# Performance work log

Measured on AMD Instinct MI355X. Metric: run time of the kernel, lower is better.

Reference implementation:

```python
import jax, jax.numpy as jnp
import numpy as np

DK = 8.0          # sqrt(in_dim) with in_dim = 64
BN_SCALE = 1.0 / np.float32(np.sqrt(1.0 + 1e-5))  # eval-mode BatchNorm3d at init (mean=0, var=1, gamma=1, beta=0)


def conv3d(x, w, b):
    # x: [B,Cin,D1,D2,D3], w: [Cout,Cin,3,3,3], stride 1, padding 1 == SAME
    y = jax.lax.conv_general_dilated(
        x, w, window_strides=(1, 1, 1), padding='SAME',
        dimension_numbers=('NCDHW', 'OIDHW', 'NCDHW'))
    return y + b[None, :, None, None, None]


def axial(qm, km, vm):
    # qm/km/vm: [B,C,S,L,M]; attention over L with keys along M-contraction.
    # scores[b,c,s,i,j] = sum_m (q/dk)[...,i,m] * k[...,j,m]  -> [B,C,S,L,L]
    s = jnp.einsum('bcsim,bcsjm->bcsij', qm / DK, km)
    # torch nn.Softmax(dim=1) applied to [N,L,L] normalizes over the FIRST L axis (i)
    a = jax.nn.softmax(s, axis=-2)
    return jnp.einsum('bcsij,bcsjm->bcsim', a, vm)


def setup_inputs() -> dict:
    key = jax.random.key(0)
    ks = jax.random.split(key, 5)
    B, C, H, W, D = 2, 64, 64, 64, 64
    x = jax.random.normal(ks[0], (B, C, H, W, D), jnp.float32)
    Wq = jax.random.normal(ks[1], (C, C, 3, 3, 3), jnp.float32) * 0.02
    Wk = jax.random.normal(ks[2], (C, C, 3, 3, 3), jnp.float32) * 0.02
    Wv = jax.random.normal(ks[3], (C, C, 3, 3, 3), jnp.float32) * 0.02
    Wc = jax.random.normal(ks[4], (C, 3 * C, 3, 3, 3), jnp.float32) * 0.02
    z = jnp.zeros((C,), jnp.float32)
    return {"x": x, "Wq": Wq, "bq": z, "Wk": Wk, "bk": z,
            "Wv": Wv, "bv": z, "Wc": Wc, "bc": z}


def reference(x, Wq, bq, Wk, bk, Wv, bv, Wc, bc):
    # projections (dropout is inactive at inference)
    q = conv3d(x, Wq, bq)
    k = conv3d(x, Wk, bk)
    v = conv3d(x, Wv, bv)
    P = jnp.transpose

    # ---- loop over D slices: attend over H (and over W in the transposed pass) ----
    pa = (0, 1, 4, 2, 3)        # [B,C,D,H,W]
    ava = axial(P(q, pa), P(k, pa), P(v, pa))          # [B,C,D,H,W]
    ava = P(ava, (0, 1, 3, 4, 2))                       # -> [B,C,H,W,D]
    pb = (0, 1, 4, 3, 2)        # [B,C,D,W,H]
    ava1 = axial(P(q, pb), P(k, pb), P(v, pb))          # [B,C,D,W,H]
    ava1 = P(ava1, (0, 1, 4, 3, 2))                     # -> [B,C,H,W,D]
    AVa = (ava + ava1) * 0.5

    # ---- loop over W slices: attend over H (and over D) ----
    pc = (0, 1, 3, 2, 4)        # [B,C,W,H,D]
    avb = axial(P(q, pc), P(k, pc), P(v, pc))           # [B,C,W,H,D]
    avb = P(avb, (0, 1, 3, 2, 4))                       # -> [B,C,H,W,D]
    pd = (0, 1, 3, 4, 2)        # [B,C,W,D,H]
    avb1 = axial(P(q, pd), P(k, pd), P(v, pd))          # [B,C,W,D,H]
    avb1 = P(avb1, (0, 1, 4, 2, 3))                     # -> [B,C,H,W,D]
    AVb = (avb + avb1) * 0.5

    # ---- loop over H slices: attend over W (and over D) ----
    avc = axial(q, k, v)                                 # [B,C,H,W,D]
    pe = (0, 1, 2, 4, 3)        # [B,C,H,D,W]
    avc1 = axial(P(q, pe), P(k, pe), P(v, pe))          # [B,C,H,D,W]
    avc1 = P(avc1, (0, 1, 2, 4, 3))                     # -> [B,C,H,W,D]
    AVc = (avc + avc1) * 0.5

    cat = jnp.concatenate([AVa, AVb, AVc], axis=1)      # [B,3C,H,W,D]
    y = jax.nn.relu(conv3d(cat, Wc, bc) * BN_SCALE)     # Conv_3x3x3: conv + BN(eval) + ReLU
    y = y * BN_SCALE                                    # outer BatchNorm3d (eval)
    return y + q
```

## Files before the change

kernel.cpp:

```cpp
#include <hip/hip_runtime.h>

typedef unsigned short u16;
typedef unsigned int u32;
typedef __attribute__((ext_vector_type(8))) __bf16 bf16x8;
typedef __attribute__((ext_vector_type(4))) float f32x4;
typedef __attribute__((ext_vector_type(4))) u16 u16x4;

#define VOL 262144

__device__ __forceinline__ u16 f2bf(float f) {
  u32 u = __builtin_bit_cast(u32, f);
  u32 r = u + 0x7FFFu + ((u >> 16) & 1u);
  return (u16)(r >> 16);
}
__device__ __forceinline__ float bf2f(u16 h) {
  return __builtin_bit_cast(float, ((u32)h) << 16);
}
__device__ __forceinline__ bf16x8 ldsfrag(const u16* p) { return *(const bf16x8*)p; }

__global__ __launch_bounds__(256) void swz_qkv(const float* __restrict__ Wq,
    const float* __restrict__ Wk, const float* __restrict__ Wv, u16* __restrict__ out) {
  int idx = blockIdx.x * 256 + threadIdx.x;
  if (idx >= 54 * 12 * 64 * 8) return;
  int jj = idx & 7;
  int lane = (idx >> 3) & 63;
  int t = idx >> 9;
  int nf = t % 12, s = t / 12;
  int dh = s / 18, sub = s % 18;
  int dw = sub / 6, dd = (sub >> 1) % 3, c32 = sub & 1;
  int coutg = nf * 16 + (lane & 15);
  int cin = c32 * 32 + (lane >> 4) * 8 + jj;
  const float* W = (coutg < 64) ? Wq : ((coutg < 128) ? Wk : Wv);
  int c = coutg & 63;
  out[idx] = f2bf(W[(c * 64 + cin) * 27 + dh * 9 + dw * 3 + dd]);
}

__global__ __launch_bounds__(256) void swz_c(const float* __restrict__ Wc, u16* __restrict__ out) {
  int idx = blockIdx.x * 256 + threadIdx.x;
  if (idx >= 162 * 4 * 64 * 8) return;
  int jj = idx & 7;
  int lane = (idx >> 3) & 63;
  int nf = (idx >> 9) & 3;
  int s = idx >> 11;
  int dh = s / 54, rem = s % 54;
  int hf = rem / 27, sub = rem % 27;
  int dw = sub / 9, dd = (sub / 3) % 3, c32 = sub % 3;
  int cout = nf * 16 + (lane & 15);
  int cin = hf * 96 + c32 * 32 + (lane >> 4) * 8 + jj;
  out[idx] = f2bf(Wc[(cout * 192 + cin) * 27 + dh * 9 + dw * 3 + dd]);
}

__global__ __launch_bounds__(256, 2) void conv_qkv(const float* __restrict__ x,
    const u16* __restrict__ BQ, const float* __restrict__ bq, const float* __restrict__ bk,
    const float* __restrict__ bv, u16* __restrict__ qb, u16* __restrict__ kb,
    u16* __restrict__ vb) {
  __shared__ __align__(16) u16 xT[4 * 66 * 72];
  int tid = threadIdx.x;
  int id = blockIdx.x;
  int lin = (id & 7) * 512 + (id >> 3);
  int b = lin >> 11, h = (lin >> 5) & 63, w0 = (lin & 31) * 2;
  int wave = tid >> 6, lane = tid & 63, r = lane & 15, g = lane >> 4;
  int pairid = tid >> 3, seg = tid & 7;
  {
    int wwi = tid >> 6, ci = tid & 63;
    xT[(wwi * 66 + 0) * 72 + ci] = 0;
    xT[(wwi * 66 + 65) * 72 + ci] = 0;
  }
  f32x4 acc[8][3];
#pragma unroll
  for (int i = 0; i < 8; ++i)
#pragma unroll
    for (int j = 0; j < 3; ++j)
#pragma unroll
      for (int e = 0; e < 4; ++e) acc[i][j][e] = 0.0f;

  for (int dh = 0; dh < 3; ++dh) {
    int hh = h + dh - 1;
    if ((unsigned)hh >= 64u) continue;
    __syncthreads();
#pragma unroll
    for (int pi = 0; pi < 4; ++pi) {
      int pair = pairid + 32 * pi;
      int wwi = pair >> 5, cin0 = (pair & 31) * 2;
      int ww = w0 + wwi - 1;
      float4 a0{}, a1{}, b0{}, b1{};
      if ((unsigned)ww < 64u) {
        const float* p = x + (size_t)(b * 64 + cin0) * VOL + hh * 4096 + ww * 64 + seg * 8;
        a0 = *(const float4*)p;        a1 = *(const float4*)(p + 4);
        b0 = *(const float4*)(p + VOL); b1 = *(const float4*)(p + VOL + 4);
      }
      u16 ua[8], ub[8];
      ua[0]=f2bf(a0.x); ua[1]=f2bf(a0.y); ua[2]=f2bf(a0.z); ua[3]=f2bf(a0.w);
      ua[4]=f2bf(a1.x); ua[5]=f2bf(a1.y); ua[6]=f2bf(a1.z); ua[7]=f2bf(a1.w);
      ub[0]=f2bf(b0.x); ub[1]=f2bf(b0.y); ub[2]=f2bf(b0.z); ub[3]=f2bf(b0.w);
      ub[4]=f2bf(b1.x); ub[5]=f2bf(b1.y); ub[6]=f2bf(b1.z); ub[7]=f2bf(b1.w);
      int basei = wwi * 66 * 72 + cin0;
#pragma unroll
      for (int di = 0; di < 8; ++di) {
        int dpos = seg * 8 + di + 1;
        *(u32*)&xT[basei + dpos * 72] = (u32)ua[di] | ((u32)ub[di] << 16);
      }
    }
    __syncthreads();
    for (int sub = 0; sub < 18; ++sub) {
      int s = dh * 18 + sub;
      int dw = sub / 6, dd = (sub >> 1) % 3, c32 = sub & 1;
      int colb = c32 * 32 + g * 8;
      bf16x8 A[8];
#pragma unroll
      for (int mf = 0; mf < 8; ++mf) {
        int wwi = (mf >> 2) + dw;
        int dpos = (mf & 3) * 16 + r + dd;
        A[mf] = ldsfrag(&xT[(wwi * 66 + dpos) * 72 + colb]);
      }
      const u16* Bp = BQ + ((size_t)(s * 12 + wave * 3) * 64 + lane) * 8;
#pragma unroll
      for (int nf = 0; nf < 3; ++nf) {
        bf16x8 Bf = *(const bf16x8*)(Bp + nf * 512);
#pragma unroll
        for (int mf = 0; mf < 8; ++mf)
          acc[mf][nf] = __builtin_amdgcn_mfma_f32_16x16x32_bf16(A[mf], Bf, acc[mf][nf], 0, 0, 0);
      }
    }
  }
#pragma unroll
  for (int nf = 0; nf < 3; ++nf) {
    int coutg = (wave * 3 + nf) * 16 + r;
    int ten = coutg >> 6, c = coutg & 63;
    u16* dst = (ten == 0) ? qb : ((ten == 1) ? kb : vb);
    const float* bias = (ten == 0) ? bq : ((ten == 1) ? bk : bv);
    float bsv = bias[c];
#pragma unroll
    for (int mf = 0; mf < 8; ++mf) {
      int wi = mf >> 2, d0 = (mf & 3) * 16 + g * 4;
      int idx = (b * 64 + c) * VOL + h * 4096 + (w0 + wi) * 64 + d0;
      u16x4 o;
#pragma unroll
      for (int jj = 0; jj < 4; ++jj) o[jj] = f2bf(acc[mf][nf][jj] + bsv);
      *(u16x4*)(dst + idx) = o;
    }
  }
}

__global__ __launch_bounds__(256, 2) void ktranspose(const u16* __restrict__ src,
    u16* __restrict__ dst, int P, int Q) {
  __shared__ __align__(16) u16 tile[64 * 72];
  int tid = threadIdx.x;
  int id = blockIdx.x;
  int bc = id >> 6, t = id & 63;
  int qt = Q >> 6;
  int p0 = (t / qt) * 64, q0 = (t % qt) * 64;
  const u16* s = src + (size_t)bc * VOL;
  u16* d = dst + (size_t)bc * VOL;
#pragma unroll
  for (int it = 0; it < 2; ++it) {
    int c = tid + 256 * it;
    int i2 = c >> 3, sg = c & 7;
    *(uint4*)&tile[i2 * 72 + sg * 8] = *(const uint4*)&s[(size_t)(p0 + i2) * Q + q0 + sg * 8];
  }
  __syncthreads();
  int j = tid >> 2, ms = tid & 3;
  u16 vals[16];
#pragma unroll
  for (int ii = 0; ii < 16; ++ii) vals[ii] = tile[(ms * 16 + ii) * 72 + j];
  uint4 o0, o1;
  o0.x = (u32)vals[0] | ((u32)vals[1] << 16);
  o0.y = (u32)vals[2] | ((u32)vals[3] << 16);
  o0.z = (u32)vals[4] | ((u32)vals[5] << 16);
  o0.w = (u32)vals[6] | ((u32)vals[7] << 16);
  o1.x = (u32)vals[8] | ((u32)vals[9] << 16);
  o1.y = (u32)vals[10] | ((u32)vals[11] << 16);
  o1.z = (u32)vals[12] | ((u32)vals[13] << 16);
  o1.w = (u32)vals[14] | ((u32)vals[15] << 16);
  size_t drow = (size_t)(q0 + j) * P + p0 + ms * 16;
  *(uint4*)&d[drow] = o0;
  *(uint4*)&d[drow + 8] = o1;
}

__global__ __launch_bounds__(256, 2) void attn_pair(const u16* __restrict__ q,
    const u16* __restrict__ k, const u16* __restrict__ v, u16* __restrict__ dst,
    int uStride, int sMul) {
  __shared__ __align__(16) u16 sm[8 * 4608];
  u16* LQ = sm;             u16* LK = sm + 4608;      u16* LV = sm + 2 * 4608;
  u16* LQT = sm + 3 * 4608; u16* LKT = sm + 4 * 4608; u16* LVT = sm + 5 * 4608;
  u16* A1 = sm + 6 * 4608;  u16* A2 = sm + 7 * 4608;
  int tid = threadIdx.x;
  int id = blockIdx.x;
  int bc = id >> 6, sidx = id & 63;
  size_t base = (size_t)bc * VOL + (size_t)sidx * sMul;
  int wave = tid >> 6, lane = tid & 63, r = lane & 15, g = lane >> 4;
  int pairid = tid >> 3, seg = tid & 7;
  int u0 = pairid * 2;
  const u16* srcs[3] = {q, k, v};
  u16* Ln_[3] = {LQ, LK, LV};
  u16* Lt_[3] = {LQT, LKT, LVT};
#pragma unroll
  for (int t3 = 0; t3 < 3; ++t3) {
    const u16* p = srcs[t3] + base + (size_t)u0 * uStride + seg * 8;
    uint4 ra = *(const uint4*)p;
    uint4 rb = *(const uint4*)(p + uStride);
    *(uint4*)&Ln_[t3][u0 * 72 + seg * 8] = ra;
    *(uint4*)&Ln_[t3][(u0 + 1) * 72 + seg * 8] = rb;
    union { uint4 vv; u16 ss[8]; } Ua, Ub;
    Ua.vv = ra; Ub.vv = rb;
#pragma unroll
    for (int vi = 0; vi < 8; ++vi) {
      int vvx = seg * 8 + vi;
      *(u32*)&Lt_[t3][vvx * 72 + u0] = (u32)Ua.ss[vi] | ((u32)Ub.ss[vi] << 16);
    }
  }
  __syncthreads();
  int row0 = wave * 16;
  f32x4 s1[4], s2[4];
#pragma unroll
  for (int nf = 0; nf < 4; ++nf)
#pragma unroll
    for (int e = 0; e < 4; ++e) { s1[nf][e] = 0.f; s2[nf][e] = 0.f; }
#pragma unroll
  for (int ks = 0; ks < 2; ++ks) {
    int cb = ks * 32 + g * 8;
    bf16x8 aK = ldsfrag(&LK[(row0 + r) * 72 + cb]);
    bf16x8 aKT = ldsfrag(&LKT[(row0 + r) * 72 + cb]);
#pragma unroll
    for (int nf = 0; nf < 4; ++nf) {
      bf16x8 bQ = ldsfrag(&LQ[(nf * 16 + r) * 72 + cb]);
      bf16x8 bQT = ldsfrag(&LQT[(nf * 16 + r) * 72 + cb]);
      s1[nf] = __builtin_amdgcn_mfma_f32_16x16x32_bf16(aK, bQ, s1[nf], 0, 0, 0);
      s2[nf] = __builtin_amdgcn_mfma_f32_16x16x32_bf16(aKT, bQT, s2[nf], 0, 0, 0);
    }
  }
#pragma unroll
  for (int m2 = 0; m2 < 2; ++m2) {
    f32x4* ss = m2 ? s2 : s1;
    u16* Adst = m2 ? A2 : A1;
#pragma unroll
    for (int jj = 0; jj < 4; ++jj) {
      float mx = fmaxf(fmaxf(ss[0][jj], ss[1][jj]), fmaxf(ss[2][jj], ss[3][jj]));
      mx = fmaxf(mx, __shfl_xor(mx, 1, 64));
      mx = fmaxf(mx, __shfl_xor(mx, 2, 64));
      mx = fmaxf(mx, __shfl_xor(mx, 4, 64));
      mx = fmaxf(mx, __shfl_xor(mx, 8, 64));
      float p0 = __expf((ss[0][jj] - mx) * 0.125f);
      float p1 = __expf((ss[1][jj] - mx) * 0.125f);
      float p2 = __expf((ss[2][jj] - mx) * 0.125f);
      float p3 = __expf((ss[3][jj] - mx) * 0.125f);
      float sum = p0 + p1 + p2 + p3;
      sum += __shfl_xor(sum, 1, 64);
      sum += __shfl_xor(sum, 2, 64);
      sum += __shfl_xor(sum, 4, 64);
      sum += __shfl_xor(sum, 8, 64);
      float inv = 1.0f / sum;
      ss[0][jj] = p0 * inv; ss[1][jj] = p1 * inv; ss[2][jj] = p2 * inv; ss[3][jj] = p3 * inv;
    }
    int j0 = row0 + g * 4;
#pragma unroll
    for (int nf = 0; nf < 4; ++nf) {
      int i = nf * 16 + r;
      *(u32*)&Adst[i * 72 + j0]     = (u32)f2bf(ss[nf][0]) | ((u32)f2bf(ss[nf][1]) << 16);
      *(u32*)&Adst[i * 72 + j0 + 2] = (u32)f2bf(ss[nf][2]) | ((u32)f2bf(ss[nf][3]) << 16);
    }
  }
  __syncthreads();
  f32x4 o[4];
#pragma unroll
  for (int nf = 0; nf < 4; ++nf)
#pragma unroll
    for (int e = 0; e < 4; ++e) o[nf][e] = 0.f;
#pragma unroll
  for (int ks = 0; ks < 2; ++ks) {
    int cb = ks * 32 + g * 8;
    bf16x8 aA = ldsfrag(&A1[(row0 + r) * 72 + cb]);
    bf16x8 aV = ldsfrag(&LV[(row0 + r) * 72 + cb]);
#pragma unroll
    for (int nf = 0; nf < 4; ++nf) {
      bf16x8 bVT = ldsfrag(&LVT[(nf * 16 + r) * 72 + cb]);
      bf16x8 bA2 = ldsfrag(&A2[(nf * 16 + r) * 72 + cb]);
      o[nf] = __builtin_amdgcn_mfma_f32_16x16x32_bf16(aA, bVT, o[nf], 0, 0, 0);
      o[nf] = __builtin_amdgcn_mfma_f32_16x16x32_bf16(aV, bA2, o[nf], 0, 0, 0);
    }
  }
#pragma unroll
  for (int nf = 0; nf < 4; ++nf) {
    int vv = nf * 16 + r;
#pragma unroll
    for (int jj = 0; jj < 4; ++jj) {
      int u = row0 + g * 4 + jj;
      dst[base + (size_t)u * uStride + vv] = f2bf(o[nf][jj] * 0.5f);
    }
  }
}

__global__ __launch_bounds__(512, 2) void conv_final(const u16* __restrict__ AVa,
    const u16* __restrict__ AVb, const u16* __restrict__ AVc, const u16* __restrict__ BCw,
    const float* __restrict__ bcb, const u16* __restrict__ qb, float* __restrict__ out) {
  __shared__ __align__(16) u16 xT[6 * 66 * 96];
  int tid = threadIdx.x;
  int id = blockIdx.x;
  int lin = (id & 7) * 256 + (id >> 3);
  int b = lin >> 10, h = (lin >> 4) & 63, w0 = (lin & 15) * 4;
  int wave = tid >> 6, lane = tid & 63, r = lane & 15, g = lane >> 4;
  int mw = wave >> 1, nw = wave & 1;
  int pairid = tid >> 3, seg = tid & 7;
  for (int z = tid; z < 576; z += 512) {
    int wwi = z / 96, ci = z % 96;
    xT[(wwi * 66 + 0) * 96 + ci] = 0;
    xT[(wwi * 66 + 65) * 96 + ci] = 0;
  }
  f32x4 acc[4][2];
#pragma unroll
  for (int i = 0; i < 4; ++i)
#pragma unroll
    for (int j = 0; j < 2; ++j)
#pragma unroll
      for (int e = 0; e < 4; ++e) acc[i][j][e] = 0.f;

  for (int dh = 0; dh < 3; ++dh) {
    int hh = h + dh - 1;
    if ((unsigned)hh >= 64u) continue;
    for (int hf = 0; hf < 2; ++hf) {
      __syncthreads();
#pragma unroll
      for (int pi = 0; pi < 5; ++pi) {
        int pair = pairid + 64 * pi;
        if (pair < 288) {
          int wwi = pair / 48;
          int cp = (pair % 48) * 2;
          int cing = hf * 96 + cp;
          int ten = cing >> 6, c = cing & 63;
          const u16* sp = (ten == 0) ? AVa : ((ten == 1) ? AVb : AVc);
          int ww = w0 + wwi - 1;
          uint4 ra{}, rb{};
          if ((unsigned)ww < 64u) {
            const u16* p = sp + (size_t)(b * 64 + c) * VOL + hh * 4096 + ww * 64 + seg * 8;
            ra = *(const uint4*)p;
            rb = *(const uint4*)(p + VOL);
          }
          union { uint4 vv; u16 ss[8]; } Ua, Ub;
          Ua.vv = ra; Ub.vv = rb;
          int basei = wwi * 66 * 96 + cp;
#pragma unroll
          for (int di = 0; di < 8; ++di) {
            int dpos = seg * 8 + di + 1;
            *(u32*)&xT[basei + dpos * 96] = (u32)Ua.ss[di] | ((u32)Ub.ss[di] << 16);
          }
        }
      }
      __syncthreads();
      for (int sub = 0; sub < 27; ++sub) {
        int s = dh * 54 + hf * 27 + sub;
        int dw = sub / 9, dd = (sub / 3) % 3, c32 = sub % 3;
        int colb = c32 * 32 + g * 8;
        int wwi = mw + dw;
        bf16x8 A[4];
#pragma unroll
        for (int dq = 0; dq < 4; ++dq) {
          int dpos = dq * 16 + r + dd;
          A[dq] = ldsfrag(&xT[(wwi * 66 + dpos) * 96 + colb]);
        }
        const u16* Bp = BCw + ((size_t)(s * 4 + nw * 2) * 64 + lane) * 8;
#pragma unroll
        for (int nf = 0; nf < 2; ++nf) {
          bf16x8 Bf = *(const bf16x8*)(Bp + nf * 512);
#pragma unroll
          for (int dq = 0; dq < 4; ++dq)
            acc[dq][nf] = __builtin_amdgcn_mfma_f32_16x16x32_bf16(A[dq], Bf, acc[dq][nf], 0, 0, 0);
        }
      }
    }
  }
  const float S = 0.9999950000374997f;
#pragma unroll
  for (int nf = 0; nf < 2; ++nf) {
    int cout = (nw * 2 + nf) * 16 + r;
    float bsv = bcb[cout];
#pragma unroll
    for (int dq = 0; dq < 4; ++dq) {
      int d0 = dq * 16 + g * 4;
      int idx = (b * 64 + cout) * VOL + h * 4096 + (w0 + mw) * 64 + d0;
      u16x4 qv = *(const u16x4*)(qb + idx);
      float4 ov;
      float t0 = (acc[dq][nf][0] + bsv) * S; t0 = t0 > 0.f ? t0 : 0.f; ov.x = t0 * S + bf2f(qv[0]);
      float t1 = (acc[dq][nf][1] + bsv) * S; t1 = t1 > 0.f ? t1 : 0.f; ov.y = t1 * S + bf2f(qv[1]);
      float t2 = (acc[dq][nf][2] + bsv) * S; t2 = t2 > 0.f ? t2 : 0.f; ov.z = t2 * S + bf2f(qv[2]);
      float t3 = (acc[dq][nf][3] + bsv) * S; t3 = t3 > 0.f ? t3 : 0.f; ov.w = t3 * S + bf2f(qv[3]);
      *(float4*)(out + idx) = ov;
    }
  }
}

extern "C" void kernel_launch(void* const* d_in, const int* in_sizes, int n_in,
                              void* d_out, int out_size, void* d_ws, size_t ws_size,
                              hipStream_t stream) {
  const float* x  = (const float*)d_in[0];
  const float* Wq = (const float*)d_in[1];
  const float* bq = (const float*)d_in[2];
  const float* Wk = (const float*)d_in[3];
  const float* bk = (const float*)d_in[4];
  const float* Wv = (const float*)d_in[5];
  const float* bv = (const float*)d_in[6];
  const float* Wc = (const float*)d_in[7];
  const float* bc = (const float*)d_in[8];
  float* out = (float*)d_out;
  u16* ws = (u16*)d_ws;
  const size_t T = (size_t)33554432;
  u16* qb = ws;
  u16* kb = ws + T;
  u16* vb = ws + 2 * T;
  u16* qT = ws + 3 * T;
  u16* kT = ws + 4 * T;
  u16* vT = ws + 5 * T;
  u16* avaT = ws + 6 * T;
  u16* BQ = ws + 7 * T;
  u16* BC = BQ + 331776;
  u16* AVa = qT;
  u16* AVb = kT;
  u16* AVc = vT;

  swz_qkv<<<1296, 256, 0, stream>>>(Wq, Wk, Wv, BQ);
  swz_c<<<1296, 256, 0, stream>>>(Wc, BC);
  conv_qkv<<<4096, 256, 0, stream>>>(x, BQ, bq, bk, bv, qb, kb, vb);
  ktranspose<<<8192, 256, 0, stream>>>(qb, qT, 4096, 64);
  ktranspose<<<8192, 256, 0, stream>>>(kb, kT, 4096, 64);
  ktranspose<<<8192, 256, 0, stream>>>(vb, vT, 4096, 64);
  attn_pair<<<8192, 256, 0, stream>>>(qT, kT, vT, avaT, 64, 4096);
  ktranspose<<<8192, 256, 0, stream>>>(avaT, AVa, 64, 4096);
  attn_pair<<<8192, 256, 0, stream>>>(qb, kb, vb, AVb, 4096, 64);
  attn_pair<<<8192, 256, 0, stream>>>(qb, kb, vb, AVc, 64, 4096);
  conv_final<<<2048, 512, 0, stream>>>(AVa, AVb, AVc, BC, bc, qb, out);
}
```

Measured before the change: 1.192 ms.

## Swizzle LDS layouts and split conv_qkv work across 8 waves

Adds XOR/rotation swizzles to the LDS tiles in conv_qkv, attn_pair and conv_final so that fragment loads and transposed stores spread across banks instead of colliding. conv_qkv now runs 512 threads, with waves split over the two w positions and four cout groups, which halves per-thread accumulators. Launch bounds are raised for conv_qkv, conv_final and ktranspose to target higher occupancy. Higher occupancy bounds may force register spills, and the swizzle adds address arithmetic.

```diff
diff --git a/kernel.cpp b/kernel.cpp
--- a/kernel.cpp
+++ b/kernel.cpp
@@ -17,6 +17,16 @@
   return __builtin_bit_cast(float, ((u32)h) << 16);
 }
 __device__ __forceinline__ bf16x8 ldsfrag(const u16* p) { return *(const bf16x8*)p; }
+
+__device__ __forceinline__ int sw72(int row, int col) {
+  return row * 72 + (col ^ (((row >> 3) & 7) << 3));
+}
+__device__ __forceinline__ int colS96(int dpos, int col) {
+  int s = ((dpos >> 1) ^ (dpos >> 3)) & 7;
+  int b = (col >> 3) + s;
+  if (b >= 12) b -= 12;
+  return (b << 3) | (col & 7);
+}
 
 __global__ __launch_bounds__(256) void swz_qkv(const float* __restrict__ Wq,
     const float* __restrict__ Wk, const float* __restrict__ Wv, u16* __restrict__ out) {
@@ -50,7 +60,7 @@
   out[idx] = f2bf(Wc[(cout * 192 + cin) * 27 + dh * 9 + dw * 3 + dd]);
 }
 
-__global__ __launch_bounds__(256, 2) void conv_qkv(const float* __restrict__ x,
+__global__ __launch_bounds__(512, 4) void conv_qkv(const float* __restrict__ x,
     const u16* __restrict__ BQ, const float* __restrict__ bq, const float* __restrict__ bk,
     const float* __restrict__ bv, u16* __restrict__ qb, u16* __restrict__ kb,
     u16* __restrict__ vb) {
@@ -60,15 +70,16 @@
   int lin = (id & 7) * 512 + (id >> 3);
   int b = lin >> 11, h = (lin >> 5) & 63, w0 = (lin & 31) * 2;
   int wave = tid >> 6, lane = tid & 63, r = lane & 15, g = lane >> 4;
+  int mhalf = wave >> 2, nq = wave & 3;
   int pairid = tid >> 3, seg = tid & 7;
-  {
+  if (tid < 256) {
     int wwi = tid >> 6, ci = tid & 63;
     xT[(wwi * 66 + 0) * 72 + ci] = 0;
     xT[(wwi * 66 + 65) * 72 + ci] = 0;
   }
-  f32x4 acc[8][3];
-#pragma unroll
-  for (int i = 0; i < 8; ++i)
+  f32x4 acc[4][3];
+#pragma unroll
+  for (int i = 0; i < 4; ++i)
 #pragma unroll
     for (int j = 0; j < 3; ++j)
 #pragma unroll
@@ -79,8 +90,8 @@
     if ((unsigned)hh >= 64u) continue;
     __syncthreads();
 #pragma unroll
-    for (int pi = 0; pi < 4; ++pi) {
-      int pair = pairid + 32 * pi;
+    for (int pi = 0; pi < 2; ++pi) {
+      int pair = pairid + 64 * pi;
       int wwi = pair >> 5, cin0 = (pair & 31) * 2;
       int ww = w0 + wwi - 1;
       float4 a0{}, a1{}, b0{}, b1{};
@@ -94,11 +105,12 @@
       ua[4]=f2bf(a1.x); ua[5]=f2bf(a1.y); ua[6]=f2bf(a1.z); ua[7]=f2bf(a1.w);
       ub[0]=f2bf(b0.x); ub[1]=f2bf(b0.y); ub[2]=f2bf(b0.z); ub[3]=f2bf(b0.w);
       ub[4]=f2bf(b1.x); ub[5]=f2bf(b1.y); ub[6]=f2bf(b1.z); ub[7]=f2bf(b1.w);
-      int basei = wwi * 66 * 72 + cin0;
+      int rowb = wwi * 66;
 #pragma unroll
       for (int di = 0; di < 8; ++di) {
         int dpos = seg * 8 + di + 1;
-        *(u32*)&xT[basei + dpos * 72] = (u32)ua[di] | ((u32)ub[di] << 16);
+        *(u32*)&xT[(rowb + dpos) * 72 + (cin0 ^ (((dpos >> 3) & 7) << 3))] =
+            (u32)ua[di] | ((u32)ub[di] << 16);
       }
     }
     __syncthreads();
@@ -106,43 +118,43 @@
       int s = dh * 18 + sub;
       int dw = sub / 6, dd = (sub >> 1) % 3, c32 = sub & 1;
       int colb = c32 * 32 + g * 8;
-      bf16x8 A[8];
-#pragma unroll
-      for (int mf = 0; mf < 8; ++mf) {
-        int wwi = (mf >> 2) + dw;
-        int dpos = (mf & 3) * 16 + r + dd;
-        A[mf] = ldsfrag(&xT[(wwi * 66 + dpos) * 72 + colb]);
-      }
-      const u16* Bp = BQ + ((size_t)(s * 12 + wave * 3) * 64 + lane) * 8;
+      int wwi = mhalf + dw;
+      bf16x8 A[4];
+#pragma unroll
+      for (int l = 0; l < 4; ++l) {
+        int dpos = l * 16 + r + dd;
+        A[l] = ldsfrag(&xT[(wwi * 66 + dpos) * 72 + (colb ^ (((dpos >> 3) & 7) << 3))]);
+      }
+      const u16* Bp = BQ + ((size_t)(s * 12 + nq * 3) * 64 + lane) * 8;
 #pragma unroll
       for (int nf = 0; nf < 3; ++nf) {
         bf16x8 Bf = *(const bf16x8*)(Bp + nf * 512);
 #pragma unroll
-        for (int mf = 0; mf < 8; ++mf)
-          acc[mf][nf] = __builtin_amdgcn_mfma_f32_16x16x32_bf16(A[mf], Bf, acc[mf][nf], 0, 0, 0);
+        for (int l = 0; l < 4; ++l)
+          acc[l][nf] = __builtin_amdgcn_mfma_f32_16x16x32_bf16(A[l], Bf, acc[l][nf], 0, 0, 0);
       }
     }
   }
 #pragma unroll
   for (int nf = 0; nf < 3; ++nf) {
-    int coutg = (wave * 3 + nf) * 16 + r;
+    int coutg = (nq * 3 + nf) * 16 + r;
     int ten = coutg >> 6, c = coutg & 63;
     u16* dst = (ten == 0) ? qb : ((ten == 1) ? kb : vb);
     const float* bias = (ten == 0) ? bq : ((ten == 1) ? bk : bv);
     float bsv = bias[c];
 #pragma unroll
-    for (int mf = 0; mf < 8; ++mf) {
-      int wi = mf >> 2, d0 = (mf & 3) * 16 + g * 4;
-      int idx = (b * 64 + c) * VOL + h * 4096 + (w0 + wi) * 64 + d0;
+    for (int l = 0; l < 4; ++l) {
+      int d0 = l * 16 + g * 4;
+      int idx = (b * 64 + c) * VOL + h * 4096 + (w0 + mhalf) * 64 + d0;
       u16x4 o;
 #pragma unroll
-      for (int jj = 0; jj < 4; ++jj) o[jj] = f2bf(acc[mf][nf][jj] + bsv);
+      for (int jj = 0; jj < 4; ++jj) o[jj] = f2bf(acc[l][nf][jj] + bsv);
       *(u16x4*)(dst + idx) = o;
     }
   }
 }
 
-__global__ __launch_bounds__(256, 2) void ktranspose(const u16* __restrict__ src,
+__global__ __launch_bounds__(256, 6) void ktranspose(const u16* __restrict__ src,
     u16* __restrict__ dst, int P, int Q) {
   __shared__ __align__(16) u16 tile[64 * 72];
   int tid = threadIdx.x;
@@ -199,14 +211,14 @@
     const u16* p = srcs[t3] + base + (size_t)u0 * uStride + seg * 8;
     uint4 ra = *(const uint4*)p;
     uint4 rb = *(const uint4*)(p + uStride);
-    *(uint4*)&Ln_[t3][u0 * 72 + seg * 8] = ra;
-    *(uint4*)&Ln_[t3][(u0 + 1) * 72 + seg * 8] = rb;
+    *(uint4*)&Ln_[t3][sw72(u0, seg * 8)] = ra;
+    *(uint4*)&Ln_[t3][sw72(u0 + 1, seg * 8)] = rb;
     union { uint4 vv; u16 ss[8]; } Ua, Ub;
     Ua.vv = ra; Ub.vv = rb;
 #pragma unroll
     for (int vi = 0; vi < 8; ++vi) {
       int vvx = seg * 8 + vi;
-      *(u32*)&Lt_[t3][vvx * 72 + u0] = (u32)Ua.ss[vi] | ((u32)Ub.ss[vi] << 16);
+      *(u32*)&Lt_[t3][sw72(vvx, u0)] = (u32)Ua.ss[vi] | ((u32)Ub.ss[vi] << 16);
     }
   }
   __syncthreads();
@@ -219,12 +231,12 @@
 #pragma unroll
   for (int ks = 0; ks < 2; ++ks) {
     int cb = ks * 32 + g * 8;
-    bf16x8 aK = ldsfrag(&LK[(row0 + r) * 72 + cb]);
-    bf16x8 aKT = ldsfrag(&LKT[(row0 + r) * 72 + cb]);
+    bf16x8 aK = ldsfrag(&LK[sw72(row0 + r, cb)]);
+    bf16x8 aKT = ldsfrag(&LKT[sw72(row0 + r, cb)]);
 #pragma unroll
     for (int nf = 0; nf < 4; ++nf) {
-      bf16x8 bQ = ldsfrag(&LQ[(nf * 16 + r) * 72 + cb]);
-      bf16x8 bQT = ldsfrag(&LQT[(nf * 16 + r) * 72 + cb]);
+      bf16x8 bQ = ldsfrag(&LQ[sw72(nf * 16 + r, cb)]);
+      bf16x8 bQT = ldsfrag(&LQT[sw72(nf * 16 + r, cb)]);
       s1[nf] = __builtin_amdgcn_mfma_f32_16x16x32_bf16(aK, bQ, s1[nf], 0, 0, 0);
       s2[nf] = __builtin_amdgcn_mfma_f32_16x16x32_bf16(aKT, bQT, s2[nf], 0, 0, 0);
     }
@@ -256,8 +268,9 @@
 #pragma unroll
     for (int nf = 0; nf < 4; ++nf) {
       int i = nf * 16 + r;
-      *(u32*)&Adst[i * 72 + j0]     = (u32)f2bf(ss[nf][0]) | ((u32)f2bf(ss[nf][1]) << 16);
-      *(u32*)&Adst[i * 72 + j0 + 2] = (u32)f2bf(ss[nf][2]) | ((u32)f2bf(ss[nf][3]) << 16);
+      int a0 = sw72(i, j0);
+      *(u32*)&Adst[a0]     = (u32)f2bf(ss[nf][0]) | ((u32)f2bf(ss[nf][1]) << 16);
+      *(u32*)&Adst[a0 + 2] = (u32)f2bf(ss[nf][2]) | ((u32)f2bf(ss[nf][3]) << 16);
     }
   }
   __syncthreads();
@@ -269,12 +282,12 @@
 #pragma unroll
   for (int ks = 0; ks < 2; ++ks) {
     int cb = ks * 32 + g * 8;
-    bf16x8 aA = ldsfrag(&A1[(row0 + r) * 72 + cb]);
-    bf16x8 aV = ldsfrag(&LV[(row0 + r) * 72 + cb]);
+    bf16x8 aA = ldsfrag(&A1[sw72(row0 + r, cb)]);
+    bf16x8 aV = ldsfrag(&LV[sw72(row0 + r, cb)]);
 #pragma unroll
     for (int nf = 0; nf < 4; ++nf) {
-      bf16x8 bVT = ldsfrag(&LVT[(nf * 16 + r) * 72 + cb]);
-      bf16x8 bA2 = ldsfrag(&A2[(nf * 16 + r) * 72 + cb]);
+      bf16x8 bVT = ldsfrag(&LVT[sw72(nf * 16 + r, cb)]);
+      bf16x8 bA2 = ldsfrag(&A2[sw72(nf * 16 + r, cb)]);
       o[nf] = __builtin_amdgcn_mfma_f32_16x16x32_bf16(aA, bVT, o[nf], 0, 0, 0);
       o[nf] = __builtin_amdgcn_mfma_f32_16x16x32_bf16(aV, bA2, o[nf], 0, 0, 0);
     }
@@ -290,7 +303,7 @@
   }
 }
 
-__global__ __launch_bounds__(512, 2) void conv_final(const u16* __restrict__ AVa,
+__global__ __launch_bounds__(512, 4) void conv_final(const u16* __restrict__ AVa,
     const u16* __restrict__ AVb, const u16* __restrict__ AVc, const u16* __restrict__ BCw,
     const float* __restrict__ bcb, const u16* __restrict__ qb, float* __restrict__ out) {
   __shared__ __align__(16) u16 xT[6 * 66 * 96];
@@ -337,11 +350,12 @@
           }
           union { uint4 vv; u16 ss[8]; } Ua, Ub;
           Ua.vv = ra; Ub.vv = rb;
-          int basei = wwi * 66 * 96 + cp;
+          int rowb = wwi * 66;
 #pragma unroll
           for (int di = 0; di < 8; ++di) {
             int dpos = seg * 8 + di + 1;
-            *(u32*)&xT[basei + dpos * 96] = (u32)Ua.ss[di] | ((u32)Ub.ss[di] << 16);
+            *(u32*)&xT[(rowb + dpos) * 96 + colS96(dpos, cp)] =
+                (u32)Ua.ss[di] | ((u32)Ub.ss[di] << 16);
           }
         }
       }
@@ -355,7 +369,7 @@
 #pragma unroll
         for (int dq = 0; dq < 4; ++dq) {
           int dpos = dq * 16 + r + dd;
-          A[dq] = ldsfrag(&xT[(wwi * 66 + dpos) * 96 + colb]);
+          A[dq] = ldsfrag(&xT[(wwi * 66 + dpos) * 96 + colS96(dpos, colb)]);
         }
         const u16* Bp = BCw + ((size_t)(s * 4 + nw * 2) * 64 + lane) * 8;
 #pragma unroll
@@ -418,7 +432,7 @@
 
   swz_qkv<<<1296, 256, 0, stream>>>(Wq, Wk, Wv, BQ);
   swz_c<<<1296, 256, 0, stream>>>(Wc, BC);
-  conv_qkv<<<4096, 256, 0, stream>>>(x, BQ, bq, bk, bv, qb, kb, vb);
+  conv_qkv<<<4096, 512, 0, stream>>>(x, BQ, bq, bk, bv, qb, kb, vb);
   ktranspose<<<8192, 256, 0, stream>>>(qb, qT, 4096, 64);
   ktranspose<<<8192, 256, 0, stream>>>(kb, kT, 4096, 64);
   ktranspose<<<8192, 256, 0, stream>>>(vb, vT, 4096, 64);
```

Measured after the change: 1.491 ms. 1.25x slower.
